# Kernel optimization log

Measured on AMD Instinct MI355X. Metric: run time of the kernel, lower is better.

## Reference

```python
import jax, jax.numpy as jnp
import numpy as np

B, L, D = 4, 896, 2048
HQ, HKV, HD = 32, 8, 64
GROUP = HQ // HKV          # 4
TOKENS_PER_FRAME = 7
ROPE_BASE = 10000.0


def setup_inputs() -> dict:
    key = jax.random.key(0)
    ks = jax.random.split(key, 5)
    s = 0.02
    return {
        "x": jax.random.normal(ks[0], (B, L, D), jnp.float32),
        "wq": jax.random.normal(ks[1], (D, D), jnp.float32) * s,
        "wk": jax.random.normal(ks[2], (D, HKV * HD), jnp.float32) * s,
        "wv": jax.random.normal(ks[3], (D, HKV * HD), jnp.float32) * s,
        "wo": jax.random.normal(ks[4], (D, D), jnp.float32) * s,
        "pos_ids": jnp.arange(L, dtype=jnp.int32),
    }


def _apply_rotary(t, cos, sin):
    # t: [B, L, H, HD]; rotate all HD dims, interleaved pairs.
    Bt, Lt, Ht, Hd = t.shape
    tp = t.reshape(Bt, Lt, Ht, Hd // 2, 2)
    x1, x2 = tp[..., 0], tp[..., 1]
    c = cos[None, :, None, :]   # [1, L, 1, HD/2]
    s = sin[None, :, None, :]
    y1 = x1 * c - x2 * s
    y2 = x1 * s + x2 * c
    return jnp.stack([y1, y2], axis=-1).reshape(Bt, Lt, Ht, Hd)


def reference(x, wq, wk, wv, wo, pos_ids):
    Bx, Lx, Dx = x.shape
    q = (x @ wq).reshape(Bx, Lx, HQ, HD)
    k = (x @ wk).reshape(Bx, Lx, HKV, HD)
    v = (x @ wv).reshape(Bx, Lx, HKV, HD)

    # RoPE (rot_dim = head_dim), scale = 1.0
    half = HD // 2
    inv_freq = 1.0 / (ROPE_BASE ** (jnp.arange(half, dtype=jnp.float32) / half))
    freqs = pos_ids.astype(jnp.float32)[:, None] * inv_freq[None, :]  # [L, HD/2]
    cos, sin = jnp.cos(freqs), jnp.sin(freqs)
    q = _apply_rotary(q, cos, sin)
    k = _apply_rotary(k, cos, sin)

    # GQA: expand kv heads to q heads (kv_head = q_head // GROUP)
    k = jnp.repeat(k, GROUP, axis=2)   # [B, L, HQ, HD]
    v = jnp.repeat(v, GROUP, axis=2)

    scale = 1.0 / jnp.sqrt(jnp.float32(HD))
    scores = jnp.einsum('blhd,bmhd->bhlm', q, k) * scale  # [B, HQ, L, L]

    # frame-block causal mask: allow key frame <= query frame
    pos = jnp.arange(Lx)
    fid = pos // TOKENS_PER_FRAME
    allow = fid[None, :] <= fid[:, None]                  # [L, L]
    neg = jnp.finfo(scores.dtype).min
    scores = jnp.where(allow[None, None], scores, neg)

    probs = jax.nn.softmax(scores, axis=-1)
    out = jnp.einsum('bhlm,bmhd->blhd', probs, v).reshape(Bx, Lx, Dx)
    return out @ wo
```

## Files before the change

kernel.cpp:

```cpp
#include <hip/hip_runtime.h>
#include <hip/hip_bf16.h>
#include <cstdint>

typedef __bf16 bf16;
typedef __bf16 bf16x8 __attribute__((ext_vector_type(8)));
typedef float floatx4 __attribute__((ext_vector_type(4)));

#define B_   4
#define L_   896
#define D_   2048
#define HQ_  32
#define HKV_ 8
#define HD_  64
#define NQKV 3072
#define M_   3584

__device__ inline void gl_lds16(const bf16* g, bf16* l) {
    __builtin_amdgcn_global_load_lds(
        (const __attribute__((address_space(1))) void*)g,
        (__attribute__((address_space(3))) void*)l, 16, 0, 0);
}

__device__ inline void barrier_() {
    asm volatile("" ::: "memory");
    __builtin_amdgcn_s_barrier();
    asm volatile("" ::: "memory");
}

__global__ __launch_bounds__(256) void rope_apply(bf16* __restrict__ QKV,
                                                  const float2* __restrict__ cs) {
    int idx = blockIdx.x * 256 + threadIdx.x;
    int m = idx / 320, g = idx - m * 320;
    int l = m % L_;
    int hp = (g * 4) & 31;
    const float2* ct = &cs[l * 32 + hp];
    bf16* p = QKV + (long)m * NQKV + g * 8;
    bf16x8 v = *(bf16x8*)p;
    bf16x8 w;
#pragma unroll
    for (int i = 0; i < 4; i++) {
        float2 csv = ct[i];
        float x1 = (float)v[2 * i], x2 = (float)v[2 * i + 1];
        w[2 * i]     = (bf16)(x1 * csv.x - x2 * csv.y);
        w[2 * i + 1] = (bf16)(x1 * csv.y + x2 * csv.x);
    }
    *(bf16x8*)p = w;
}

__device__ inline void tr_cvt_body(const float* __restrict__ in,
                                   ushort* __restrict__ out, int C, int R,
                                   int bx, int by, int tid, ushort (*t)[72]) {
    int tr = tid >> 4, tc = (tid & 15) << 2;
    long r0 = (long)by << 6, c0 = (long)bx << 6;
#pragma unroll
    for (int i = 0; i < 4; ++i) {
        float4 v = *(const float4*)&in[(r0 + tr + i * 16) * C + c0 + tc];
        union { bf16 b[4]; ushort4 u; } w;
        w.b[0] = (bf16)v.x; w.b[1] = (bf16)v.y; w.b[2] = (bf16)v.z; w.b[3] = (bf16)v.w;
        *(ushort4*)&t[tr + i * 16][tc] = w.u;
    }
    __syncthreads();
#pragma unroll
    for (int i = 0; i < 4; ++i) {
        ushort4 w;
        w.x = t[tc + 0][tr + i * 16];
        w.y = t[tc + 1][tr + i * 16];
        w.z = t[tc + 2][tr + i * 16];
        w.w = t[tc + 3][tr + i * 16];
        *(ushort4*)&out[(c0 + tr + i * 16) * R + r0 + tc] = w;
    }
}

__global__ __launch_bounds__(256) void prep_kernel(
    const float* __restrict__ x, const float* __restrict__ wq,
    const float* __restrict__ wk, const float* __restrict__ wv,
    const float* __restrict__ wo, const int* __restrict__ pos_ids,
    bf16* __restrict__ xb, bf16* __restrict__ wqkvT, bf16* __restrict__ woT,
    float2* __restrict__ cs) {
    __shared__ ushort t[64][72];
    const int d = blockIdx.x, tid = threadIdx.x;
    if (d < 7168) {
        long q = (long)d * 256 + tid;
        float4 v = ((const float4*)x)[q];
        union { bf16 b[4]; ushort4 u; } w;
        w.b[0] = (bf16)v.x; w.b[1] = (bf16)v.y; w.b[2] = (bf16)v.z; w.b[3] = (bf16)v.w;
        ((ushort4*)xb)[q] = w.u;
    } else if (d < 8192) {
        int e = d - 7168;
        tr_cvt_body(wq, (ushort*)wqkvT, 2048, 2048, e & 31, e >> 5, tid, t);
    } else if (d < 9216) {
        int e = d - 8192;
        tr_cvt_body(wo, (ushort*)woT, 2048, 2048, e & 31, e >> 5, tid, t);
    } else if (d < 9472) {
        int e = d - 9216;
        tr_cvt_body(wk, (ushort*)(wqkvT + 4194304L), 512, 2048, e & 7, e >> 3, tid, t);
    } else if (d < 9728) {
        int e = d - 9472;
        tr_cvt_body(wv, (ushort*)(wqkvT + 5242880L), 512, 2048, e & 7, e >> 3, tid, t);
    } else {
        int idx = (d - 9728) * 256 + tid;
        if (idx < L_ * 32) {
            int l = idx >> 5, i = idx & 31;
            float p = (float)pos_ids[l];
            float inv = exp2f(-(float)i * (13.287712379549449f / 32.0f));
            float a = p * inv;
            cs[idx] = make_float2(cosf(a), sinf(a));
        }
    }
}

__global__ __launch_bounds__(256) void transpose_u16(
    const ushort* __restrict__ in, ushort* __restrict__ out,
    int ld_in, int ld_out, long is1, long is2, long os1, long os2) {
    __shared__ ushort t[64][72];
    int z = blockIdx.z;
    const ushort* ip = in + (long)(z >> 3) * is1 + (long)(z & 7) * is2;
    ushort* op = out + (long)(z >> 3) * os1 + (long)(z & 7) * os2;
    int tid = threadIdx.x;
    int tr = tid >> 4, tc = (tid & 15) << 2;
    long r0 = (long)blockIdx.y << 6, c0 = (long)blockIdx.x << 6;
#pragma unroll
    for (int i = 0; i < 4; ++i) {
        ushort4 v = *(const ushort4*)&ip[(r0 + tr + i * 16) * ld_in + c0 + tc];
        *(ushort4*)&t[tr + i * 16][tc] = v;
    }
    __syncthreads();
#pragma unroll
    for (int i = 0; i < 4; ++i) {
        ushort4 w;
        w.x = t[tc + 0][tr + i * 16];
        w.y = t[tc + 1][tr + i * 16];
        w.z = t[tc + 2][tr + i * 16];
        w.w = t[tc + 3][tr + i * 16];
        *(ushort4*)&op[(c0 + tr + i * 16) * ld_out + r0 + tc] = w;
    }
}

template <int JF, int OUTF32>
__global__ __launch_bounds__(512, 2) void gemm224(
    const bf16* __restrict__ A, const bf16* __restrict__ Bt, void* __restrict__ C,
    int Ntot, int Ktot) {
    __shared__ bf16 ldsA[2][224 * 64];
    __shared__ bf16 ldsB[2][JF * 64 * 64];
    const int tid = threadIdx.x;
    const int lane = tid & 63;
    const int quad = lane >> 4, l16 = lane & 15;
    const int w = tid >> 6;
    const int wr = w >> 2, wc = w & 3;

    const int gx = gridDim.x;
    const int nwg = gx * gridDim.y;
    int orig = blockIdx.y * gx + blockIdx.x;
    int q8 = nwg >> 3, r8 = nwg & 7;
    int xcd = orig & 7, lid = orig >> 3;
    int wg = (xcd < r8 ? xcd * (q8 + 1) : r8 * (q8 + 1) + (xcd - r8) * q8) + lid;
    const long m0 = (long)(wg / gx) * 224;
    const long n0 = (long)(wg % gx) * (JF * 64);

    const long rowK = Ktot;
    const int srow = tid >> 3;
    const int scol = ((tid & 7) ^ (srow & 7)) << 3;
    const bf16* baseA = A  + (m0 + srow) * rowK + scol;
    const bf16* baseB = Bt + (n0 + srow) * rowK + scol;
    bf16* const dA = (bf16*)ldsA + tid * 8;
    bf16* const dB = (bf16*)ldsB + tid * 8;

    const int m7 = l16 & 7;
    const int col0 = ((0 + quad) ^ m7) << 3;
    const int col1 = ((4 + quad) ^ m7) << 3;
    const int abase = wr * 112 + l16;
    const int bbase = wc * (JF * 16) + l16;

    floatx4 acc[7][JF];
#pragma unroll
    for (int i = 0; i < 7; ++i)
#pragma unroll
        for (int j = 0; j < JF; ++j)
#pragma unroll
            for (int r = 0; r < 4; ++r) acc[i][j][r] = 0.f;

    bf16x8 af0[4][2], af1[3][2], bq[JF][2];

    const int T = Ktot >> 6;

    {
        gl_lds16(baseA,              dA);
        gl_lds16(baseA + 64 * rowK,  dA + 4096);
        gl_lds16(baseA + 128 * rowK, dA + 8192);
        if (tid < 256) gl_lds16(baseA + 192 * rowK, dA + 12288);
#pragma unroll
        for (int r = 0; r < JF; ++r) gl_lds16(baseB + r * 64 * rowK, dB + r * 4096);
#pragma unroll
        for (int r = 0; r < JF; ++r) gl_lds16(baseB + 64 + r * 64 * rowK,
                                              dB + JF * 4096 + r * 4096);
    }
    if (JF == 3) asm volatile("s_waitcnt vmcnt(3)" ::: "memory");
    else         asm volatile("s_waitcnt vmcnt(2)" ::: "memory");
    barrier_();

    for (int t = 0; t < T; ++t) {
        const int cur = t & 1, nxt = cur ^ 1;
        const bf16* pa = &ldsA[cur][0];
        const bf16* pb = &ldsB[cur][0];
        const long koff  = (long)(t + 1) * 64;
        const long koff2 = (long)(t + 2) * 64;

#pragma unroll
        for (int i = 0; i < 4; ++i) {
            const bf16* rp = &pa[(abase + i * 16) * 64];
            af0[i][0] = *(const bf16x8*)&rp[col0];
            af0[i][1] = *(const bf16x8*)&rp[col1];
        }
#pragma unroll
        for (int j = 0; j < JF; ++j) {
            const bf16* rp = &pb[(bbase + j * 16) * 64];
            bq[j][0] = *(const bf16x8*)&rp[col0];
            bq[j][1] = *(const bf16x8*)&rp[col1];
        }
        if (t + 1 < T) {
            const bf16* g = baseA + koff;
            bf16* l = dA + nxt * (224 * 64);
            gl_lds16(g,              l);
            gl_lds16(g + 64 * rowK,  l + 4096);
            gl_lds16(g + 128 * rowK, l + 8192);
            if (tid < 256) gl_lds16(g + 192 * rowK, l + 12288);
        }
        barrier_();
        asm volatile("s_waitcnt lgkmcnt(0)" ::: "memory");
        __builtin_amdgcn_sched_barrier(0);
        __builtin_amdgcn_s_setprio(1);
#pragma unroll
        for (int i = 0; i < 4; ++i)
#pragma unroll
            for (int j = 0; j < JF; ++j) {
                floatx4 c = acc[i][j];
                c = __builtin_amdgcn_mfma_f32_16x16x32_bf16(af0[i][0], bq[j][0], c, 0, 0, 0);
                c = __builtin_amdgcn_mfma_f32_16x16x32_bf16(af0[i][1], bq[j][1], c, 0, 0, 0);
                acc[i][j] = c;
            }
        __builtin_amdgcn_s_setprio(0);
        barrier_();

#pragma unroll
        for (int i = 0; i < 3; ++i) {
            const bf16* rp = &pa[(abase + (4 + i) * 16) * 64];
            af1[i][0] = *(const bf16x8*)&rp[col0];
            af1[i][1] = *(const bf16x8*)&rp[col1];
        }
        if (t + 2 < T) {
            const bf16* g = baseB + koff2;
            bf16* l = dB + cur * (JF * 64 * 64);
#pragma unroll
            for (int r = 0; r < JF; ++r) gl_lds16(g + r * 64 * rowK, l + r * 4096);
        }
        barrier_();
        asm volatile("s_waitcnt lgkmcnt(0)" ::: "memory");
        __builtin_amdgcn_sched_barrier(0);
        __builtin_amdgcn_s_setprio(1);
#pragma unroll
        for (int i = 0; i < 3; ++i)
#pragma unroll
            for (int j = 0; j < JF; ++j) {
                floatx4 c = acc[4 + i][j];
                c = __builtin_amdgcn_mfma_f32_16x16x32_bf16(af1[i][0], bq[j][0], c, 0, 0, 0);
                c = __builtin_amdgcn_mfma_f32_16x16x32_bf16(af1[i][1], bq[j][1], c, 0, 0, 0);
                acc[4 + i][j] = c;
            }
        __builtin_amdgcn_s_setprio(0);
        if (t + 2 < T) {
            if (JF == 3) asm volatile("s_waitcnt vmcnt(3)" ::: "memory");
            else         asm volatile("s_waitcnt vmcnt(2)" ::: "memory");
        } else {
            asm volatile("s_waitcnt vmcnt(0)" ::: "memory");
        }
        barrier_();
    }

#pragma unroll
    for (int i = 0; i < 7; ++i)
#pragma unroll
        for (int j = 0; j < JF; ++j)
#pragma unroll
            for (int r = 0; r < 4; ++r) {
                long m = m0 + wr * 112 + i * 16 + quad * 4 + r;
                long n = n0 + wc * (JF * 16) + j * 16 + l16;
                if (OUTF32) ((float*)C)[m * Ntot + n] = acc[i][j][r];
                else        ((bf16*)C)[m * Ntot + n] = (bf16)acc[i][j][r];
            }
}

__global__ __launch_bounds__(256) void attn_kernel(
    const bf16* __restrict__ QKV,
    const bf16* __restrict__ Vt,
    bf16* __restrict__ AO) {
    __shared__ bf16 Ks[64 * 64];
    __shared__ bf16 Vs[64 * 64];
    const int tid  = threadIdx.x;
    const int lane = tid & 63;
    const int wid  = tid >> 6;
    const int quad = lane >> 4, c = lane & 15;
    const int b = blockIdx.z;
    const int kvh = blockIdx.y >> 1, hp = blockIdx.y & 1;
    const int hq = kvh * 4 + hp * 2 + (wid >> 1);
    const int sub = wid & 1;
    const int xpair = blockIdx.x;

    const bf16* Kb = QKV + ((long)(b * L_)) * NQKV + D_ + kvh * HD_;
    const bf16* Vb = Vt + ((long)(b * HKV_ + kvh)) * (HD_ * L_);

    const int srow = tid >> 3, schunk = (tid & 7) << 3;
    const int sslot = ((tid & 7) ^ (srow & 7)) << 3;
    const bf16* kp0 = &Kb[(long)srow * NQKV + schunk];
    const bf16* kp1 = &Kb[(long)(32 + srow) * NQKV + schunk];
    const bf16* vp0 = &Vb[(long)srow * L_ + schunk];
    const bf16* vp1 = &Vb[(long)(srow + 32) * L_ + schunk];

    const int m7 = c & 7;
    const int col0 = ((0 + quad) ^ m7) << 3;
    const int col1 = ((4 + quad) ^ m7) << 3;

    const int srcA = ((quad & 1) << 5) + c;
    const int srcB = srcA + 16;
    const int nsel = quad >> 1;

    const floatx4 fzero = {0.f, 0.f, 0.f, 0.f};
    const float C1 = 0.18033688011112042f;

#pragma unroll 1
    for (int pass = 0; pass < 2; ++pass) {
        const int x = pass == 0 ? xpair : 13 - xpair;
        const int q0b = x * 64;
        const bf16* Qb = QKV + ((long)(b * L_ + q0b + sub * 32)) * NQKV + hq * HD_;

        bf16x8 qf[2][2];
#pragma unroll
        for (int a = 0; a < 2; a++) {
            qf[a][0] = *(const bf16x8*)&Qb[(long)(a * 16 + c) * NQKV + quad * 8];
            qf[a][1] = *(const bf16x8*)&Qb[(long)(a * 16 + c) * NQKV + 32 + quad * 8];
        }

        float lsum[2];
        floatx4 o[2][4];
#pragma unroll
        for (int a = 0; a < 2; a++) {
            lsum[a] = 0.f;
#pragma unroll
            for (int nt = 0; nt < 4; nt++)
#pragma unroll
                for (int r = 0; r < 4; r++) o[a][nt][r] = 0.f;
        }

        int fe[2];
#pragma unroll
        for (int a = 0; a < 2; a++) {
            int l = q0b + sub * 32 + a * 16 + c;
            fe[a] = (l / 7 + 1) * 7;
        }
        const int femin = (q0b / 7 + 1) * 7;
        const int kend  = ((q0b + 63) / 7 + 1) * 7;

        bf16x8 kg0 = *(const bf16x8*)&kp0[0];
        bf16x8 kg1 = *(const bf16x8*)&kp1[0];
        bf16x8 vg0 = *(const bf16x8*)&vp0[0];
        bf16x8 vg1 = *(const bf16x8*)&vp1[0];

        for (int k0 = 0; k0 < kend; k0 += 64) {
            __syncthreads();
            *(bf16x8*)&Ks[srow * 64 + sslot]        = kg0;
            *(bf16x8*)&Ks[(srow + 32) * 64 + sslot] = kg1;
            *(bf16x8*)&Vs[srow * 64 + sslot]        = vg0;
            *(bf16x8*)&Vs[(srow + 32) * 64 + sslot] = vg1;
            __syncthreads();

            const int kn = k0 + 64;
            if (kn < kend) {
                kg0 = *(const bf16x8*)&kp0[(long)kn * NQKV];
                kg1 = *(const bf16x8*)&kp1[(long)kn * NQKV];
                vg0 = *(const bf16x8*)&vp0[kn];
                vg1 = *(const bf16x8*)&vp1[kn];
            }

            bf16x8 kf[4][2];
#pragma unroll
            for (int n = 0; n < 4; n++) {
                const bf16* rp = &Ks[(n * 16 + c) * 64];
                kf[n][0] = *(bf16x8*)&rp[col0];
                kf[n][1] = *(bf16x8*)&rp[col1];
            }
            bf16x8 vf[4][2];
#pragma unroll
            for (int nt = 0; nt < 4; nt++) {
                const bf16* rp = &Vs[(nt * 16 + c) * 64];
                vf[nt][0] = *(bf16x8*)&rp[col0];
                vf[nt][1] = *(bf16x8*)&rp[col1];
            }
            const int masked = (k0 + 64 > femin);
#pragma unroll
            for (int a = 0; a < 2; a++) {
                floatx4 s[4];
#pragma unroll
                for (int n = 0; n < 4; n++) {
                    s[n] = __builtin_amdgcn_mfma_f32_16x16x32_bf16(kf[n][0], qf[a][0], fzero, 0, 0, 0);
                    s[n] = __builtin_amdgcn_mfma_f32_16x16x32_bf16(kf[n][1], qf[a][1], s[n], 0, 0, 0);
                }
                float e[4][4];
                if (masked) {
#pragma unroll
                    for (int n = 0; n < 4; n++)
#pragma unroll
                        for (int r = 0; r < 4; r++) {
                            const int key = k0 + n * 16 + quad * 4 + r;
                            float v = exp2f(s[n][r] * C1);
                            v = (key < fe[a]) ? v : 0.f;
                            e[n][r] = v;
                            lsum[a] += v;
                        }
                } else {
#pragma unroll
                    for (int n = 0; n < 4; n++)
#pragma unroll
                        for (int r = 0; r < 4; r++) {
                            float v = exp2f(s[n][r] * C1);
                            e[n][r] = v;
                            lsum[a] += v;
                        }
                }
                uint pk[4][2];
#pragma unroll
                for (int n = 0; n < 4; n++) {
                    union { bf16 h[2]; uint u; } t0, t1;
                    t0.h[0] = (bf16)e[n][0]; t0.h[1] = (bf16)e[n][1];
                    t1.h[0] = (bf16)e[n][2]; t1.h[1] = (bf16)e[n][3];
                    pk[n][0] = t0.u; pk[n][1] = t1.u;
                }
                union { uint u[4]; bf16x8 v; } pf0, pf1;
                {
                    uint a0 = __shfl((int)pk[0][0], srcA);
                    uint a1 = __shfl((int)pk[1][0], srcA);
                    pf0.u[0] = nsel ? a1 : a0;
                    uint b0 = __shfl((int)pk[0][1], srcA);
                    uint b1 = __shfl((int)pk[1][1], srcA);
                    pf0.u[1] = nsel ? b1 : b0;
                    uint c0_ = __shfl((int)pk[0][0], srcB);
                    uint c1_ = __shfl((int)pk[1][0], srcB);
                    pf0.u[2] = nsel ? c1_ : c0_;
                    uint d0 = __shfl((int)pk[0][1], srcB);
                    uint d1 = __shfl((int)pk[1][1], srcB);
                    pf0.u[3] = nsel ? d1 : d0;
                    uint e0 = __shfl((int)pk[2][0], srcA);
                    uint e1 = __shfl((int)pk[3][0], srcA);
                    pf1.u[0] = nsel ? e1 : e0;
                    uint f0 = __shfl((int)pk[2][1], srcA);
                    uint f1 = __shfl((int)pk[3][1], srcA);
                    pf1.u[1] = nsel ? f1 : f0;
                    uint g0 = __shfl((int)pk[2][0], srcB);
                    uint g1 = __shfl((int)pk[3][0], srcB);
                    pf1.u[2] = nsel ? g1 : g0;
                    uint h0 = __shfl((int)pk[2][1], srcB);
                    uint h1 = __shfl((int)pk[3][1], srcB);
                    pf1.u[3] = nsel ? h1 : h0;
                }
#pragma unroll
                for (int nt = 0; nt < 4; nt++) {
                    o[a][nt] = __builtin_amdgcn_mfma_f32_16x16x32_bf16(pf0.v, vf[nt][0], o[a][nt], 0, 0, 0);
                    o[a][nt] = __builtin_amdgcn_mfma_f32_16x16x32_bf16(pf1.v, vf[nt][1], o[a][nt], 0, 0, 0);
                }
            }
        }
#pragma unroll
        for (int a = 0; a < 2; a++) {
            lsum[a] += __shfl_xor(lsum[a], 16);
            lsum[a] += __shfl_xor(lsum[a], 32);
        }
#pragma unroll
        for (int a = 0; a < 2; a++)
#pragma unroll
            for (int r = 0; r < 4; r++) {
                float ls = __shfl(lsum[a], (lane & 48) + quad * 4 + r);
                int l = q0b + sub * 32 + a * 16 + quad * 4 + r;
#pragma unroll
                for (int nt = 0; nt < 4; nt++)
                    AO[((long)(b * L_ + l)) * D_ + hq * HD_ + nt * 16 + c] =
                        (bf16)(o[a][nt][r] / ls);
            }
    }
}

extern "C" void kernel_launch(void* const* d_in, const int* in_sizes, int n_in,
                              void* d_out, int out_size, void* d_ws, size_t ws_size,
                              hipStream_t stream) {
    (void)in_sizes; (void)n_in; (void)out_size; (void)ws_size;
    const float* x  = (const float*)d_in[0];
    const float* wq = (const float*)d_in[1];
    const float* wk = (const float*)d_in[2];
    const float* wv = (const float*)d_in[3];
    const float* wo = (const float*)d_in[4];
    const int* pos  = (const int*)d_in[5];

    bf16* ws    = (bf16*)d_ws;
    bf16* xb    = ws;
    bf16* wqkvT = ws + 7340032L;
    bf16* woT   = ws + 13631488L;
    bf16* QKV   = ws + 17825792L;
    bf16* Vt    = ws + 28835840L;
    bf16* AO    = xb;
    float2* cs  = (float2*)(ws + 30670848L);

    prep_kernel<<<dim3(9840), 256, 0, stream>>>(x, wq, wk, wv, wo, pos,
                                                xb, wqkvT, woT, cs);

    gemm224<3, 0><<<dim3(16, 16), 512, 0, stream>>>(xb, wqkvT, QKV, NQKV, D_);

    rope_apply<<<dim3(4480), 256, 0, stream>>>(QKV, cs);

    transpose_u16<<<dim3(1, 14, 32), 256, 0, stream>>>(
        (const ushort*)(QKV + 2560), (ushort*)Vt, 3072, 896,
        896L * 3072, 64, 8L * 57344, 57344);

    attn_kernel<<<dim3(7, 16, 4), 256, 0, stream>>>(QKV, Vt, AO);

    gemm224<2, 1><<<dim3(16, 16), 512, 0, stream>>>(AO, woT, d_out, D_, D_);
}
```

Before: 251.3 us.

## Merge rope and V-transpose kernels; split attention pair loop into separate blocks

The RoPE application and the V transpose are merged into one launch, with block ranges dispatched by blockIdx. This is safe because the transpose reads only the V columns, which RoPE does not touch. The attention kernel no longer processes two query tiles per block (balanced pairing x and 13-x). Instead it launches 14 tiles per head, scheduled heaviest-first, which doubles the grid from 448 to 896 blocks. The goal is to save a launch and raise parallelism, at the risk of load imbalance compared with the paired scheme.

```diff
diff --git a/kernel.cpp b/kernel.cpp
--- a/kernel.cpp
+++ b/kernel.cpp
@@ -25,26 +25,6 @@
     asm volatile("" ::: "memory");
     __builtin_amdgcn_s_barrier();
     asm volatile("" ::: "memory");
-}
-
-__global__ __launch_bounds__(256) void rope_apply(bf16* __restrict__ QKV,
-                                                  const float2* __restrict__ cs) {
-    int idx = blockIdx.x * 256 + threadIdx.x;
-    int m = idx / 320, g = idx - m * 320;
-    int l = m % L_;
-    int hp = (g * 4) & 31;
-    const float2* ct = &cs[l * 32 + hp];
-    bf16* p = QKV + (long)m * NQKV + g * 8;
-    bf16x8 v = *(bf16x8*)p;
-    bf16x8 w;
-#pragma unroll
-    for (int i = 0; i < 4; i++) {
-        float2 csv = ct[i];
-        float x1 = (float)v[2 * i], x2 = (float)v[2 * i + 1];
-        w[2 * i]     = (bf16)(x1 * csv.x - x2 * csv.y);
-        w[2 * i + 1] = (bf16)(x1 * csv.y + x2 * csv.x);
-    }
-    *(bf16x8*)p = w;
 }
 
 __device__ inline void tr_cvt_body(const float* __restrict__ in,
@@ -109,30 +89,51 @@
     }
 }
 
-__global__ __launch_bounds__(256) void transpose_u16(
-    const ushort* __restrict__ in, ushort* __restrict__ out,
-    int ld_in, int ld_out, long is1, long is2, long os1, long os2) {
+__global__ __launch_bounds__(256) void post_kernel(
+    bf16* __restrict__ QKV, const float2* __restrict__ cs,
+    ushort* __restrict__ Vt) {
     __shared__ ushort t[64][72];
-    int z = blockIdx.z;
-    const ushort* ip = in + (long)(z >> 3) * is1 + (long)(z & 7) * is2;
-    ushort* op = out + (long)(z >> 3) * os1 + (long)(z & 7) * os2;
-    int tid = threadIdx.x;
-    int tr = tid >> 4, tc = (tid & 15) << 2;
-    long r0 = (long)blockIdx.y << 6, c0 = (long)blockIdx.x << 6;
-#pragma unroll
-    for (int i = 0; i < 4; ++i) {
-        ushort4 v = *(const ushort4*)&ip[(r0 + tr + i * 16) * ld_in + c0 + tc];
-        *(ushort4*)&t[tr + i * 16][tc] = v;
-    }
-    __syncthreads();
-#pragma unroll
-    for (int i = 0; i < 4; ++i) {
-        ushort4 w;
-        w.x = t[tc + 0][tr + i * 16];
-        w.y = t[tc + 1][tr + i * 16];
-        w.z = t[tc + 2][tr + i * 16];
-        w.w = t[tc + 3][tr + i * 16];
-        *(ushort4*)&op[(c0 + tr + i * 16) * ld_out + r0 + tc] = w;
+    const int d = blockIdx.x, tid = threadIdx.x;
+    if (d < 4480) {
+        int idx = d * 256 + tid;
+        int m = idx / 320, g = idx - m * 320;
+        int l = m % L_;
+        int hp = (g * 4) & 31;
+        const float2* ct = &cs[l * 32 + hp];
+        bf16* p = QKV + (long)m * NQKV + g * 8;
+        bf16x8 v = *(bf16x8*)p;
+        bf16x8 w;
+#pragma unroll
+        for (int i = 0; i < 4; i++) {
+            float2 csv = ct[i];
+            float x1 = (float)v[2 * i], x2 = (float)v[2 * i + 1];
+            w[2 * i]     = (bf16)(x1 * csv.x - x2 * csv.y);
+            w[2 * i + 1] = (bf16)(x1 * csv.y + x2 * csv.x);
+        }
+        *(bf16x8*)p = w;
+    } else {
+        const int e = d - 4480;
+        const int by = e % 14, z = e / 14;
+        const ushort* ip = (const ushort*)(QKV + 2560)
+                           + (long)(z >> 3) * (896L * 3072) + (long)(z & 7) * 64;
+        ushort* op = Vt + (long)(z >> 3) * (8L * 57344) + (long)(z & 7) * 57344;
+        int tr = tid >> 4, tc = (tid & 15) << 2;
+        long r0 = (long)by << 6, c0 = 0;
+#pragma unroll
+        for (int i = 0; i < 4; ++i) {
+            ushort4 v = *(const ushort4*)&ip[(r0 + tr + i * 16) * 3072 + c0 + tc];
+            *(ushort4*)&t[tr + i * 16][tc] = v;
+        }
+        __syncthreads();
+#pragma unroll
+        for (int i = 0; i < 4; ++i) {
+            ushort4 w;
+            w.x = t[tc + 0][tr + i * 16];
+            w.y = t[tc + 1][tr + i * 16];
+            w.z = t[tc + 2][tr + i * 16];
+            w.w = t[tc + 3][tr + i * 16];
+            *(ushort4*)&op[(c0 + tr + i * 16) * 896 + r0 + tc] = w;
+        }
     }
 }
 
@@ -303,7 +304,7 @@
     const int kvh = blockIdx.y >> 1, hp = blockIdx.y & 1;
     const int hq = kvh * 4 + hp * 2 + (wid >> 1);
     const int sub = wid & 1;
-    const int xpair = blockIdx.x;
+    const int x = 13 - blockIdx.x;
 
     const bf16* Kb = QKV + ((long)(b * L_)) * NQKV + D_ + kvh * HD_;
     const bf16* Vb = Vt + ((long)(b * HKV_ + kvh)) * (HD_ * L_);
@@ -326,164 +327,160 @@
     const floatx4 fzero = {0.f, 0.f, 0.f, 0.f};
     const float C1 = 0.18033688011112042f;
 
-#pragma unroll 1
-    for (int pass = 0; pass < 2; ++pass) {
-        const int x = pass == 0 ? xpair : 13 - xpair;
-        const int q0b = x * 64;
-        const bf16* Qb = QKV + ((long)(b * L_ + q0b + sub * 32)) * NQKV + hq * HD_;
-
-        bf16x8 qf[2][2];
+    const int q0b = x * 64;
+    const bf16* Qb = QKV + ((long)(b * L_ + q0b + sub * 32)) * NQKV + hq * HD_;
+
+    bf16x8 qf[2][2];
+#pragma unroll
+    for (int a = 0; a < 2; a++) {
+        qf[a][0] = *(const bf16x8*)&Qb[(long)(a * 16 + c) * NQKV + quad * 8];
+        qf[a][1] = *(const bf16x8*)&Qb[(long)(a * 16 + c) * NQKV + 32 + quad * 8];
+    }
+
+    float lsum[2];
+    floatx4 o[2][4];
+#pragma unroll
+    for (int a = 0; a < 2; a++) {
+        lsum[a] = 0.f;
+#pragma unroll
+        for (int nt = 0; nt < 4; nt++)
+#pragma unroll
+            for (int r = 0; r < 4; r++) o[a][nt][r] = 0.f;
+    }
+
+    int fe[2];
+#pragma unroll
+    for (int a = 0; a < 2; a++) {
+        int l = q0b + sub * 32 + a * 16 + c;
+        fe[a] = (l / 7 + 1) * 7;
+    }
+    const int femin = (q0b / 7 + 1) * 7;
+    const int kend  = ((q0b + 63) / 7 + 1) * 7;
+
+    bf16x8 kg0 = *(const bf16x8*)&kp0[0];
+    bf16x8 kg1 = *(const bf16x8*)&kp1[0];
+    bf16x8 vg0 = *(const bf16x8*)&vp0[0];
+    bf16x8 vg1 = *(const bf16x8*)&vp1[0];
+
+    for (int k0 = 0; k0 < kend; k0 += 64) {
+        __syncthreads();
+        *(bf16x8*)&Ks[srow * 64 + sslot]        = kg0;
+        *(bf16x8*)&Ks[(srow + 32) * 64 + sslot] = kg1;
+        *(bf16x8*)&Vs[srow * 64 + sslot]        = vg0;
+        *(bf16x8*)&Vs[(srow + 32) * 64 + sslot] = vg1;
+        __syncthreads();
+
+        const int kn = k0 + 64;
+        if (kn < kend) {
+            kg0 = *(const bf16x8*)&kp0[(long)kn * NQKV];
+            kg1 = *(const bf16x8*)&kp1[(long)kn * NQKV];
+            vg0 = *(const bf16x8*)&vp0[kn];
+            vg1 = *(const bf16x8*)&vp1[kn];
+        }
+
+        bf16x8 kf[4][2];
+#pragma unroll
+        for (int n = 0; n < 4; n++) {
+            const bf16* rp = &Ks[(n * 16 + c) * 64];
+            kf[n][0] = *(bf16x8*)&rp[col0];
+            kf[n][1] = *(bf16x8*)&rp[col1];
+        }
+        bf16x8 vf[4][2];
+#pragma unroll
+        for (int nt = 0; nt < 4; nt++) {
+            const bf16* rp = &Vs[(nt * 16 + c) * 64];
+            vf[nt][0] = *(bf16x8*)&rp[col0];
+            vf[nt][1] = *(bf16x8*)&rp[col1];
+        }
+        const int masked = (k0 + 64 > femin);
 #pragma unroll
         for (int a = 0; a < 2; a++) {
-            qf[a][0] = *(const bf16x8*)&Qb[(long)(a * 16 + c) * NQKV + quad * 8];
-            qf[a][1] = *(const bf16x8*)&Qb[(long)(a * 16 + c) * NQKV + 32 + quad * 8];
-        }
-
-        float lsum[2];
-        floatx4 o[2][4];
-#pragma unroll
-        for (int a = 0; a < 2; a++) {
-            lsum[a] = 0.f;
+            floatx4 s[4];
+#pragma unroll
+            for (int n = 0; n < 4; n++) {
+                s[n] = __builtin_amdgcn_mfma_f32_16x16x32_bf16(kf[n][0], qf[a][0], fzero, 0, 0, 0);
+                s[n] = __builtin_amdgcn_mfma_f32_16x16x32_bf16(kf[n][1], qf[a][1], s[n], 0, 0, 0);
+            }
+            float e[4][4];
+            if (masked) {
+#pragma unroll
+                for (int n = 0; n < 4; n++)
+#pragma unroll
+                    for (int r = 0; r < 4; r++) {
+                        const int key = k0 + n * 16 + quad * 4 + r;
+                        float v = exp2f(s[n][r] * C1);
+                        v = (key < fe[a]) ? v : 0.f;
+                        e[n][r] = v;
+                        lsum[a] += v;
+                    }
+            } else {
+#pragma unroll
+                for (int n = 0; n < 4; n++)
+#pragma unroll
+                    for (int r = 0; r < 4; r++) {
+                        float v = exp2f(s[n][r] * C1);
+                        e[n][r] = v;
+                        lsum[a] += v;
+                    }
+            }
+            uint pk[4][2];
+#pragma unroll
+            for (int n = 0; n < 4; n++) {
+                union { bf16 h[2]; uint u; } t0, t1;
+                t0.h[0] = (bf16)e[n][0]; t0.h[1] = (bf16)e[n][1];
+                t1.h[0] = (bf16)e[n][2]; t1.h[1] = (bf16)e[n][3];
+                pk[n][0] = t0.u; pk[n][1] = t1.u;
+            }
+            union { uint u[4]; bf16x8 v; } pf0, pf1;
+            {
+                uint a0 = __shfl((int)pk[0][0], srcA);
+                uint a1 = __shfl((int)pk[1][0], srcA);
+                pf0.u[0] = nsel ? a1 : a0;
+                uint b0 = __shfl((int)pk[0][1], srcA);
+                uint b1 = __shfl((int)pk[1][1], srcA);
+                pf0.u[1] = nsel ? b1 : b0;
+                uint c0_ = __shfl((int)pk[0][0], srcB);
+                uint c1_ = __shfl((int)pk[1][0], srcB);
+                pf0.u[2] = nsel ? c1_ : c0_;
+                uint d0 = __shfl((int)pk[0][1], srcB);
+                uint d1 = __shfl((int)pk[1][1], srcB);
+                pf0.u[3] = nsel ? d1 : d0;
+                uint e0 = __shfl((int)pk[2][0], srcA);
+                uint e1 = __shfl((int)pk[3][0], srcA);
+                pf1.u[0] = nsel ? e1 : e0;
+                uint f0 = __shfl((int)pk[2][1], srcA);
+                uint f1 = __shfl((int)pk[3][1], srcA);
+                pf1.u[1] = nsel ? f1 : f0;
+                uint g0 = __shfl((int)pk[2][0], srcB);
+                uint g1 = __shfl((int)pk[3][0], srcB);
+                pf1.u[2] = nsel ? g1 : g0;
+                uint h0 = __shfl((int)pk[2][1], srcB);
+                uint h1 = __shfl((int)pk[3][1], srcB);
+                pf1.u[3] = nsel ? h1 : h0;
+            }
+#pragma unroll
+            for (int nt = 0; nt < 4; nt++) {
+                o[a][nt] = __builtin_amdgcn_mfma_f32_16x16x32_bf16(pf0.v, vf[nt][0], o[a][nt], 0, 0, 0);
+                o[a][nt] = __builtin_amdgcn_mfma_f32_16x16x32_bf16(pf1.v, vf[nt][1], o[a][nt], 0, 0, 0);
+            }
+        }
+    }
+#pragma unroll
+    for (int a = 0; a < 2; a++) {
+        lsum[a] += __shfl_xor(lsum[a], 16);
+        lsum[a] += __shfl_xor(lsum[a], 32);
+    }
+#pragma unroll
+    for (int a = 0; a < 2; a++)
+#pragma unroll
+        for (int r = 0; r < 4; r++) {
+            float ls = __shfl(lsum[a], (lane & 48) + quad * 4 + r);
+            int l = q0b + sub * 32 + a * 16 + quad * 4 + r;
 #pragma unroll
             for (int nt = 0; nt < 4; nt++)
-#pragma unroll
-                for (int r = 0; r < 4; r++) o[a][nt][r] = 0.f;
-        }
-
-        int fe[2];
-#pragma unroll
-        for (int a = 0; a < 2; a++) {
-            int l = q0b + sub * 32 + a * 16 + c;
-            fe[a] = (l / 7 + 1) * 7;
-        }
-        const int femin = (q0b / 7 + 1) * 7;
-        const int kend  = ((q0b + 63) / 7 + 1) * 7;
-
-        bf16x8 kg0 = *(const bf16x8*)&kp0[0];
-        bf16x8 kg1 = *(const bf16x8*)&kp1[0];
-        bf16x8 vg0 = *(const bf16x8*)&vp0[0];
-        bf16x8 vg1 = *(const bf16x8*)&vp1[0];
-
-        for (int k0 = 0; k0 < kend; k0 += 64) {
-            __syncthreads();
-            *(bf16x8*)&Ks[srow * 64 + sslot]        = kg0;
-            *(bf16x8*)&Ks[(srow + 32) * 64 + sslot] = kg1;
-            *(bf16x8*)&Vs[srow * 64 + sslot]        = vg0;
-            *(bf16x8*)&Vs[(srow + 32) * 64 + sslot] = vg1;
-            __syncthreads();
-
-            const int kn = k0 + 64;
-            if (kn < kend) {
-                kg0 = *(const bf16x8*)&kp0[(long)kn * NQKV];
-                kg1 = *(const bf16x8*)&kp1[(long)kn * NQKV];
-                vg0 = *(const bf16x8*)&vp0[kn];
-                vg1 = *(const bf16x8*)&vp1[kn];
-            }
-
-            bf16x8 kf[4][2];
-#pragma unroll
-            for (int n = 0; n < 4; n++) {
-                const bf16* rp = &Ks[(n * 16 + c) * 64];
-                kf[n][0] = *(bf16x8*)&rp[col0];
-                kf[n][1] = *(bf16x8*)&rp[col1];
-            }
-            bf16x8 vf[4][2];
-#pragma unroll
-            for (int nt = 0; nt < 4; nt++) {
-                const bf16* rp = &Vs[(nt * 16 + c) * 64];
-                vf[nt][0] = *(bf16x8*)&rp[col0];
-                vf[nt][1] = *(bf16x8*)&rp[col1];
-            }
-            const int masked = (k0 + 64 > femin);
-#pragma unroll
-            for (int a = 0; a < 2; a++) {
-                floatx4 s[4];
-#pragma unroll
-                for (int n = 0; n < 4; n++) {
-                    s[n] = __builtin_amdgcn_mfma_f32_16x16x32_bf16(kf[n][0], qf[a][0], fzero, 0, 0, 0);
-                    s[n] = __builtin_amdgcn_mfma_f32_16x16x32_bf16(kf[n][1], qf[a][1], s[n], 0, 0, 0);
-                }
-                float e[4][4];
-                if (masked) {
-#pragma unroll
-                    for (int n = 0; n < 4; n++)
-#pragma unroll
-                        for (int r = 0; r < 4; r++) {
-                            const int key = k0 + n * 16 + quad * 4 + r;
-                            float v = exp2f(s[n][r] * C1);
-                            v = (key < fe[a]) ? v : 0.f;
-                            e[n][r] = v;
-                            lsum[a] += v;
-                        }
-                } else {
-#pragma unroll
-                    for (int n = 0; n < 4; n++)
-#pragma unroll
-                        for (int r = 0; r < 4; r++) {
-                            float v = exp2f(s[n][r] * C1);
-                            e[n][r] = v;
-                            lsum[a] += v;
-                        }
-                }
-                uint pk[4][2];
-#pragma unroll
-                for (int n = 0; n < 4; n++) {
-                    union { bf16 h[2]; uint u; } t0, t1;
-                    t0.h[0] = (bf16)e[n][0]; t0.h[1] = (bf16)e[n][1];
-                    t1.h[0] = (bf16)e[n][2]; t1.h[1] = (bf16)e[n][3];
-                    pk[n][0] = t0.u; pk[n][1] = t1.u;
-                }
-                union { uint u[4]; bf16x8 v; } pf0, pf1;
-                {
-                    uint a0 = __shfl((int)pk[0][0], srcA);
-                    uint a1 = __shfl((int)pk[1][0], srcA);
-                    pf0.u[0] = nsel ? a1 : a0;
-                    uint b0 = __shfl((int)pk[0][1], srcA);
-                    uint b1 = __shfl((int)pk[1][1], srcA);
-                    pf0.u[1] = nsel ? b1 : b0;
-                    uint c0_ = __shfl((int)pk[0][0], srcB);
-                    uint c1_ = __shfl((int)pk[1][0], srcB);
-                    pf0.u[2] = nsel ? c1_ : c0_;
-                    uint d0 = __shfl((int)pk[0][1], srcB);
-                    uint d1 = __shfl((int)pk[1][1], srcB);
-                    pf0.u[3] = nsel ? d1 : d0;
-                    uint e0 = __shfl((int)pk[2][0], srcA);
-                    uint e1 = __shfl((int)pk[3][0], srcA);
-                    pf1.u[0] = nsel ? e1 : e0;
-                    uint f0 = __shfl((int)pk[2][1], srcA);
-                    uint f1 = __shfl((int)pk[3][1], srcA);
-                    pf1.u[1] = nsel ? f1 : f0;
-                    uint g0 = __shfl((int)pk[2][0], srcB);
-                    uint g1 = __shfl((int)pk[3][0], srcB);
-                    pf1.u[2] = nsel ? g1 : g0;
-                    uint h0 = __shfl((int)pk[2][1], srcB);
-                    uint h1 = __shfl((int)pk[3][1], srcB);
-                    pf1.u[3] = nsel ? h1 : h0;
-                }
-#pragma unroll
-                for (int nt = 0; nt < 4; nt++) {
-                    o[a][nt] = __builtin_amdgcn_mfma_f32_16x16x32_bf16(pf0.v, vf[nt][0], o[a][nt], 0, 0, 0);
-                    o[a][nt] = __builtin_amdgcn_mfma_f32_16x16x32_bf16(pf1.v, vf[nt][1], o[a][nt], 0, 0, 0);
-                }
-            }
-        }
-#pragma unroll
-        for (int a = 0; a < 2; a++) {
-            lsum[a] += __shfl_xor(lsum[a], 16);
-            lsum[a] += __shfl_xor(lsum[a], 32);
-        }
-#pragma unroll
-        for (int a = 0; a < 2; a++)
-#pragma unroll
-            for (int r = 0; r < 4; r++) {
-                float ls = __shfl(lsum[a], (lane & 48) + quad * 4 + r);
-                int l = q0b + sub * 32 + a * 16 + quad * 4 + r;
-#pragma unroll
-                for (int nt = 0; nt < 4; nt++)
-                    AO[((long)(b * L_ + l)) * D_ + hq * HD_ + nt * 16 + c] =
-                        (bf16)(o[a][nt][r] / ls);
-            }
-    }
+                AO[((long)(b * L_ + l)) * D_ + hq * HD_ + nt * 16 + c] =
+                    (bf16)(o[a][nt][r] / ls);
+        }
 }
 
 extern "C" void kernel_launch(void* const* d_in, const int* in_sizes, int n_in,
@@ -511,13 +508,9 @@
 
     gemm224<3, 0><<<dim3(16, 16), 512, 0, stream>>>(xb, wqkvT, QKV, NQKV, D_);
 
-    rope_apply<<<dim3(4480), 256, 0, stream>>>(QKV, cs);
-
-    transpose_u16<<<dim3(1, 14, 32), 256, 0, stream>>>(
-        (const ushort*)(QKV + 2560), (ushort*)Vt, 3072, 896,
-        896L * 3072, 64, 8L * 57344, 57344);
-
-    attn_kernel<<<dim3(7, 16, 4), 256, 0, stream>>>(QKV, Vt, AO);
+    post_kernel<<<dim3(4928), 256, 0, stream>>>(QKV, cs, (ushort*)Vt);
+
+    attn_kernel<<<dim3(14, 16, 4), 256, 0, stream>>>(QKV, Vt, AO);
 
     gemm224<2, 1><<<dim3(16, 16), 512, 0, stream>>>(AO, woT, d_out, D_, D_);
 }
```

New measurement: 261.7 us. 4.2% more time.
